# Kernel tuning notes

Hardware: AMD Instinct MI355X
Metric: run time of the kernel (lower is better)

## Reference

```python
import jax, jax.numpy as jnp
import numpy as np

N_DOMAINS = 8
LN_EPS = 1e-5


def setup_inputs() -> dict:
    key = jax.random.key(0)
    ks = jax.random.split(key, 4)
    N, D_IN, D_HID, D_OUT = 32768, 256, 1024, 256
    x = jax.random.normal(ks[0], (N, D_IN), dtype=jnp.float32)
    domain_types = jax.random.randint(ks[1], (N,), 0, N_DOMAINS, dtype=jnp.int32)
    # Per-domain MLP parameters (8 independent experts)
    W1 = jax.random.normal(ks[2], (N_DOMAINS, D_IN, D_HID), dtype=jnp.float32) * (1.0 / np.sqrt(D_IN))
    b1 = jnp.zeros((N_DOMAINS, D_HID), dtype=jnp.float32)
    gamma = jnp.ones((N_DOMAINS, D_HID), dtype=jnp.float32)
    beta = jnp.zeros((N_DOMAINS, D_HID), dtype=jnp.float32)
    W2 = jax.random.normal(ks[3], (N_DOMAINS, D_HID, D_OUT), dtype=jnp.float32) * (1.0 / np.sqrt(D_HID))
    b2 = jnp.zeros((N_DOMAINS, D_OUT), dtype=jnp.float32)
    return {"x": x, "domain_types": domain_types, "W1": W1, "b1": b1,
            "gamma": gamma, "beta": beta, "W2": W2, "b2": b2}


def _expert_mlp(x, W1d, b1d, gd, bd, W2d, b2d):
    # Linear -> LayerNorm -> ReLU -> (Dropout: identity at eval) -> Linear
    h = x @ W1d + b1d                       # [N, hid]
    mu = jnp.mean(h, axis=-1, keepdims=True)
    var = jnp.mean(jnp.square(h - mu), axis=-1, keepdims=True)
    h = (h - mu) * jax.lax.rsqrt(var + LN_EPS) * gd + bd
    h = jax.nn.relu(h)
    return h @ W2d + b2d                    # [N, out]


def reference(x, domain_types, W1, b1, gamma, beta, W2, b2):
    # output dim == x.shape[-1] (as in the torch code: zeros(batch, x.shape[-1]))
    out = jnp.zeros((x.shape[0], x.shape[-1]), dtype=x.dtype)
    for d in range(N_DOMAINS):  # small fixed expert loop (static MoE dispatch)
        y = _expert_mlp(x, W1[d], b1[d], gamma[d], beta[d], W2[d], b2[d])
        mask = (domain_types == d)[:, None]
        out = jnp.where(mask, y, out)
    return out
```

## Files before the change

kernel.cpp:

```cpp
#include <hip/hip_runtime.h>
#include <hip/hip_bf16.h>


#define ND 8
#define NROWS 32768
#define DIN 256
#define DHID 1024
#define DOUT 256
#define MPAD 33792
#define NTILES 264

typedef short short8 __attribute__((ext_vector_type(8)));
typedef float floatx4 __attribute__((ext_vector_type(4)));

__device__ __forceinline__ unsigned short f2bf(float f) {
    unsigned u = __builtin_bit_cast(unsigned, f);
    unsigned r = u + 0x7fff + ((u >> 16) & 1);
    return (unsigned short)(r >> 16);
}
__device__ __forceinline__ float bf2f(unsigned short h) {
    unsigned u = ((unsigned)h) << 16;
    return __builtin_bit_cast(float, u);
}

#define GLDS16(gp, lp) __builtin_amdgcn_global_load_lds( \
    (const __attribute__((address_space(1))) void*)(gp), \
    (__attribute__((address_space(3))) void*)(lp), 16, 0, 0)

__global__ void transpose_both(const float* __restrict__ W1, unsigned short* __restrict__ W1T,
                               const float* __restrict__ W2, unsigned short* __restrict__ W2T,
                               int* __restrict__ cnt) {
    if (blockIdx.x == 0 && threadIdx.x < 16) cnt[threadIdx.x] = 0;
    __shared__ float t[32][33];
    int b = blockIdx.x;
    const float* in; unsigned short* out; int R, C, bx, by, z;
    if (b < 2048) {
        in = W1; out = W1T; R = DIN; C = DHID;
        bx = b & 31; by = (b >> 5) & 7; z = b >> 8;
    } else {
        b -= 2048;
        in = W2; out = W2T; R = DHID; C = DOUT;
        bx = b & 7; by = (b >> 3) & 31; z = b >> 8;
    }
    const int c0 = bx * 32, r0 = by * 32;
    const int tx = threadIdx.x & 31, ty = threadIdx.x >> 5;
    const float* src = in + (size_t)z * R * C;
    unsigned short* dst = out + (size_t)z * R * C;
#pragma unroll
    for (int i = 0; i < 32; i += 8)
        t[ty + i][tx] = src[(size_t)(r0 + ty + i) * C + c0 + tx];
    __syncthreads();
#pragma unroll
    for (int i = 0; i < 32; i += 8)
        dst[(size_t)(c0 + ty + i) * R + r0 + tx] = f2bf(t[tx][ty + i]);
}

__global__ void init_histo(const int* __restrict__ dt, int* __restrict__ perm,
                           int* __restrict__ counts) {
    const int i = blockIdx.x * 256 + threadIdx.x;
    if (i < MPAD) perm[i] = -1;
    __shared__ int lc[ND];
    if (threadIdx.x < ND) lc[threadIdx.x] = 0;
    __syncthreads();
    if (i < NROWS) atomicAdd(&lc[dt[i]], 1);
    __syncthreads();
    if (threadIdx.x < ND && lc[threadIdx.x] > 0)
        atomicAdd(&counts[threadIdx.x], lc[threadIdx.x]);
}

__global__ void make_meta(const int* __restrict__ counts, int* __restrict__ cursors,
                          int2* __restrict__ meta) {
    __shared__ int base[ND], ntc[ND];
    const int t = threadIdx.x;
    if (t == 0) {
        int off = 0;
        for (int d = 0; d < ND; d++) {
            base[d] = off;
            ntc[d] = (counts[d] + 127) >> 7;
            cursors[d] = off;
            off += ntc[d] << 7;
        }
    }
    __syncthreads();
    for (int i = t; i < NTILES; i += 64) {
        int2 m = make_int2(-1, 0);
#pragma unroll
        for (int d = 0; d < ND; d++) {
            const int ti = i - (base[d] >> 7);
            if (ti >= 0 && ti < ntc[d]) m = make_int2(d, base[d] + (ti << 7));
        }
        meta[i] = m;
    }
}

__global__ __launch_bounds__(256)
void assign_pos(const int* __restrict__ dt, int* __restrict__ cursors,
                int* __restrict__ perm, int* __restrict__ pos) {
    __shared__ int lcnt[ND];
    __shared__ int lbase[ND];
    const int tid = threadIdx.x;
    if (tid < ND) lcnt[tid] = 0;
    __syncthreads();
    const int r = blockIdx.x * 256 + tid;
    const int d = dt[r];
    const int myrank = atomicAdd(&lcnt[d], 1);
    __syncthreads();
    if (tid < ND && lcnt[tid] > 0)
        lbase[tid] = atomicAdd(&cursors[tid], lcnt[tid]);
    __syncthreads();
    const int p = lbase[d] + myrank;
    pos[r] = p;
    perm[p] = r;
}

__global__ __launch_bounds__(256)
void copy_rows(const float* __restrict__ x, const int* __restrict__ pos,
               unsigned short* __restrict__ xs) {
    const int tid = threadIdx.x;
    const int lane = tid & 63;
    const int r = blockIdx.x * 4 + (tid >> 6);
    const int p = pos[r];
    float4 v = ((const float4*)(x + (size_t)r * DIN))[lane];
    ushort4 o;
    o.x = f2bf(v.x); o.y = f2bf(v.y); o.z = f2bf(v.z); o.w = f2bf(v.w);
    ((ushort4*)(xs + (size_t)p * DIN))[lane] = o;
}

template <int K, bool ISB>
__global__ __launch_bounds__(256, 2)
void gemm_bt(const unsigned short* __restrict__ A,
             const unsigned short* __restrict__ Bt,
             const float* __restrict__ bias,
             const int2* __restrict__ meta,
             const int* __restrict__ perm,
             unsigned short* __restrict__ Cbf,
             float* __restrict__ Cf,
             const int Ntot,
             float2* __restrict__ spart,
             const float* __restrict__ gamma,
             const float* __restrict__ beta) {
    constexpr int NB = ISB ? 2 : 8;
    constexpr int NWG = NTILES * NB;
    constexpr int NS = K / 32;
    const int bid = (int)blockIdx.x;
    const int wid = (bid & 7) * (NWG >> 3) + (bid >> 3);
    const int tile = wid / NB;
    const int n0 = (wid % NB) * 128;
    const int2 md = meta[tile];
    const int dom = md.x;
    if (dom < 0) return;
    const int m0 = md.y;

    __shared__ unsigned short As[2][128 * 32];
    __shared__ unsigned short Bs[2][128 * 32];
    __shared__ float gb[ISB ? 2048 : 64];
    __shared__ float sred[2][128];

    const int tid = threadIdx.x;
    const int lane = tid & 63;
    const int w = tid >> 6;
    const int wr = w >> 1, wc = w & 1;
    const int l15 = lane & 15;

    const unsigned short* Abase = A + (size_t)m0 * K;
    const unsigned short* Bbase = Bt + (size_t)dom * Ntot * K + (size_t)n0 * K;

    if (!ISB) {
        if (tid < 128) { sred[0][tid] = 0.f; sred[1][tid] = 0.f; }
    }

    const int ma = (w * 128 + lane) >> 2;
    const int kc = lane & 3;
    float muv[2], rsv[2];
    short8 hv0{}, hv1{};
    if (ISB) {
        ((float4*)gb)[tid] = ((const float4*)(gamma + dom * DHID))[tid];
        ((float4*)(gb + 1024))[tid] = ((const float4*)(beta + dom * DHID))[tid];
#pragma unroll
        for (int h2 = 0; h2 < 2; ++h2) {
            const int rm = m0 + ma + h2 * 16;
            float s = 0.f, s2 = 0.f;
#pragma unroll
            for (int nb = 0; nb < 8; ++nb) {
                const float2 p = spart[(size_t)nb * MPAD + rm];
                s += p.x; s2 += p.y;
            }
            const float mu = s * (1.f / 1024.f);
            const float var = fmaxf(s2 * (1.f / 1024.f) - mu * mu, 0.f);
            muv[h2] = mu;
            rsv[h2] = rsqrtf(var + 1e-5f);
        }
        hv0 = *(const short8*)(Abase + (size_t)ma * K + kc * 8);
        hv1 = *(const short8*)(Abase + (size_t)(ma + 16) * K + kc * 8);
    }

#define STAGE_B(buf, t_) {                                                     \
        const int k0_ = (t_) * 32;                                             \
        _Pragma("unroll")                                                      \
        for (int it = 0; it < 2; ++it) {                                       \
            const int c = w * 128 + it * 64 + lane;                            \
            const int m_ = c >> 2, kcc = c & 3;                                \
            GLDS16(Bbase + (size_t)m_ * K + k0_ + kcc * 8,                     \
                   &Bs[buf][(w * 128 + it * 64) * 8]);                         \
        }                                                                      \
    }
#define STAGE_A_GLDS(buf, t_) {                                                \
        const int k0_ = (t_) * 32;                                             \
        _Pragma("unroll")                                                      \
        for (int it = 0; it < 2; ++it) {                                       \
            const int c = w * 128 + it * 64 + lane;                            \
            const int m_ = c >> 2, kcc = c & 3;                                \
            GLDS16(Abase + (size_t)m_ * K + k0_ + kcc * 8,                     \
                   &As[buf][(w * 128 + it * 64) * 8]);                         \
        }                                                                      \
    }
#define STAGE_A_XFRM(buf, t_) {                                                \
        const int k1 = (t_) * 32 + kc * 8;                                     \
        const float4 g0 = *(const float4*)&gb[k1];                             \
        const float4 g1 = *(const float4*)&gb[k1 + 4];                         \
        const float4 e0 = *(const float4*)&gb[1024 + k1];                      \
        const float4 e1 = *(const float4*)&gb[1024 + k1 + 4];                  \
        const float gA[8] = {g0.x, g0.y, g0.z, g0.w, g1.x, g1.y, g1.z, g1.w};  \
        const float eA[8] = {e0.x, e0.y, e0.z, e0.w, e1.x, e1.y, e1.z, e1.w};  \
        _Pragma("unroll")                                                      \
        for (int h2 = 0; h2 < 2; ++h2) {                                       \
            const float mu = muv[h2], rs = rsv[h2];                            \
            const short8 hvv = h2 ? hv1 : hv0;                                 \
            short8 o;                                                          \
            _Pragma("unroll")                                                  \
            for (int e = 0; e < 8; ++e) {                                      \
                const float rg = gA[e] * rs;                                   \
                const float v = fmaxf(fmaf(bf2f((unsigned short)hvv[e]), rg,   \
                                           fmaf(-mu, rg, eA[e])), 0.f);        \
                o[e] = (short)f2bf(v);                                         \
            }                                                                  \
            *(short8*)&As[buf][(w * 128 + h2 * 64 + lane) * 8] = o;            \
        }                                                                      \
    }
#define LOAD_H(t_) {                                                           \
        const int k0_ = (t_) * 32;                                             \
        hv0 = *(const short8*)(Abase + (size_t)ma * K + k0_ + kc * 8);         \
        hv1 = *(const short8*)(Abase + (size_t)(ma + 16) * K + k0_ + kc * 8);  \
    }

    floatx4 acc[4][4];
#pragma unroll
    for (int i = 0; i < 4; i++)
#pragma unroll
        for (int j = 0; j < 4; j++) acc[i][j] = 0.f;

    STAGE_B(0, 0)
    if (!ISB) {
        STAGE_A_GLDS(0, 0)
    } else {
        STAGE_A_XFRM(0, 0)
        LOAD_H(1)
    }
    __syncthreads();

    int cur = 0;
    const int kk = (lane >> 4) * 8;
    for (int t = 0; t < NS - 1; ++t) {
        const int nx = cur ^ 1;
        STAGE_B(nx, t + 1)
        if (!ISB) {
            STAGE_A_GLDS(nx, t + 1)
        } else {
            STAGE_A_XFRM(nx, t + 1)
            if (t + 2 < NS) LOAD_H(t + 2)
        }
        short8 a[4], b[4];
#pragma unroll
        for (int i = 0; i < 4; i++) {
            const int m = wr * 64 + i * 16 + l15;
            a[i] = *(const short8*)&As[cur][m * 32 + kk];
            const int n = wc * 64 + i * 16 + l15;
            b[i] = *(const short8*)&Bs[cur][n * 32 + kk];
        }
        __builtin_amdgcn_s_setprio(1);
#pragma unroll
        for (int i = 0; i < 4; i++)
#pragma unroll
            for (int j = 0; j < 4; j++)
                acc[i][j] = __builtin_amdgcn_mfma_f32_16x16x32_bf16(a[i], b[j], acc[i][j], 0, 0, 0);
        __builtin_amdgcn_s_setprio(0);
        __syncthreads();
        cur = nx;
    }
    {
        short8 a[4], b[4];
#pragma unroll
        for (int i = 0; i < 4; i++) {
            const int m = wr * 64 + i * 16 + l15;
            a[i] = *(const short8*)&As[cur][m * 32 + kk];
            const int n = wc * 64 + i * 16 + l15;
            b[i] = *(const short8*)&Bs[cur][n * 32 + kk];
        }
        __builtin_amdgcn_s_setprio(1);
#pragma unroll
        for (int i = 0; i < 4; i++)
#pragma unroll
            for (int j = 0; j < 4; j++)
                acc[i][j] = __builtin_amdgcn_mfma_f32_16x16x32_bf16(a[i], b[j], acc[i][j], 0, 0, 0);
        __builtin_amdgcn_s_setprio(0);
    }
#undef STAGE_B
#undef STAGE_A_GLDS
#undef STAGE_A_XFRM
#undef LOAD_H

    const int quad = lane >> 4;
    if (!ISB) {
        float bv[4];
#pragma unroll
        for (int j = 0; j < 4; j++)
            bv[j] = bias[dom * Ntot + n0 + wc * 64 + j * 16 + l15];
#pragma unroll
        for (int i = 0; i < 4; i++) {
#pragma unroll
            for (int r = 0; r < 4; r++) {
                const int rl = wr * 64 + i * 16 + quad * 4 + r;
                float s = 0.f, s2 = 0.f;
#pragma unroll
                for (int j = 0; j < 4; j++) {
                    const float v = acc[i][j][r] + bv[j];
                    Cbf[(size_t)(m0 + rl) * Ntot + n0 + wc * 64 + j * 16 + l15] = f2bf(v);
                    s += v; s2 += v * v;
                }
#pragma unroll
                for (int o = 8; o; o >>= 1) {
                    s  += __shfl_xor(s, o, 64);
                    s2 += __shfl_xor(s2, o, 64);
                }
                if (l15 == 0) {
                    atomicAdd(&sred[0][rl], s);
                    atomicAdd(&sred[1][rl], s2);
                }
            }
        }
        __syncthreads();
        if (tid < 128)
            spart[(size_t)(n0 >> 7) * MPAD + m0 + tid] =
                make_float2(sred[0][tid], sred[1][tid]);
    } else {
#pragma unroll
        for (int i = 0; i < 4; i++) {
            const int rowbase = m0 + wr * 64 + i * 16 + quad * 4;
#pragma unroll
            for (int r = 0; r < 4; r++) {
                const int orig = perm[rowbase + r];
                if (orig < 0) continue;
#pragma unroll
                for (int j = 0; j < 4; j++) {
                    const int col = n0 + wc * 64 + j * 16 + l15;
                    Cf[(size_t)orig * Ntot + col] = acc[i][j][r] + bias[dom * Ntot + col];
                }
            }
        }
    }
}

extern "C" void kernel_launch(void* const* d_in, const int* in_sizes, int n_in,
                              void* d_out, int out_size, void* d_ws, size_t ws_size,
                              hipStream_t stream) {
    const float* x = (const float*)d_in[0];
    const int* dt = (const int*)d_in[1];
    const float* W1 = (const float*)d_in[2];
    const float* b1 = (const float*)d_in[3];
    const float* gamma = (const float*)d_in[4];
    const float* beta = (const float*)d_in[5];
    const float* W2 = (const float*)d_in[6];
    const float* b2 = (const float*)d_in[7];
    float* out = (float*)d_out;

    char* ws = (char*)d_ws;
    size_t off = 0;
    auto take = [&](size_t nbytes) -> char* {
        char* p = ws + off;
        off = (off + nbytes + 255) & ~(size_t)255;
        return p;
    };
    unsigned short* W1T = (unsigned short*)take((size_t)ND * DHID * DIN * 2);
    unsigned short* W2T = (unsigned short*)take((size_t)ND * DOUT * DHID * 2);
    unsigned short* XS  = (unsigned short*)take((size_t)MPAD * DIN * 2);
    unsigned short* H   = (unsigned short*)take((size_t)MPAD * DHID * 2);
    float2* SPART = (float2*)take((size_t)8 * MPAD * 8);
    int* PERM   = (int*)take(MPAD * 4);
    int* POS    = (int*)take(NROWS * 4);
    int* CNT    = (int*)take(64);
    int2* META  = (int2*)take(NTILES * 8);
    (void)ws_size; (void)n_in; (void)in_sizes; (void)out_size;

    int* COUNTS = CNT;
    int* CURSORS = CNT + 8;

    transpose_both<<<4096, 256, 0, stream>>>(W1, W1T, W2, W2T, CNT);
    init_histo<<<MPAD / 256, 256, 0, stream>>>(dt, PERM, COUNTS);
    make_meta<<<1, 64, 0, stream>>>(COUNTS, CURSORS, META);
    assign_pos<<<NROWS / 256, 256, 0, stream>>>(dt, CURSORS, PERM, POS);
    copy_rows<<<NROWS / 4, 256, 0, stream>>>(x, POS, XS);
    gemm_bt<DIN, false><<<NTILES * 8, 256, 0, stream>>>(
        XS, W1T, b1, META, nullptr, H, nullptr, DHID, SPART, nullptr, nullptr);
    gemm_bt<DHID, true><<<NTILES * 2, 256, 0, stream>>>(
        H, W2T, b2, META, PERM, nullptr, out, DOUT, SPART, gamma, beta);
}
```

Baseline: 201.6 us.

## Fuse preprocessing into cooperative kernel and use K=64 swizzled second GEMM

The five small preprocessing kernels (weight transpose, histogram, metadata, position assignment, row copy) are merged into one cooperative kernel that uses grid-wide syncs, cutting launch overhead and the gaps between launches. The second GEMM becomes a dedicated kernel with a 64-wide K step and an XOR-swizzled LDS layout, and W2T is written pre-swizzled to match. This halves the number of K iterations and barriers and is meant to cut LDS bank conflicts. In exchange, the prep phase runs on only 256 blocks and pays for grid.sync, and the larger LDS tiles may lower occupancy.

```diff
diff --git a/kernel.cpp b/kernel.cpp
--- a/kernel.cpp
+++ b/kernel.cpp
@@ -1,6 +1,9 @@
 #include <hip/hip_runtime.h>
 #include <hip/hip_bf16.h>
-
+#include <hip/hip_cooperative_groups.h>
+
+
+namespace cg = cooperative_groups;
 
 #define ND 8
 #define NROWS 32768
@@ -27,121 +30,122 @@
     (const __attribute__((address_space(1))) void*)(gp), \
     (__attribute__((address_space(3))) void*)(lp), 16, 0, 0)
 
-__global__ void transpose_both(const float* __restrict__ W1, unsigned short* __restrict__ W1T,
-                               const float* __restrict__ W2, unsigned short* __restrict__ W2T,
-                               int* __restrict__ cnt) {
-    if (blockIdx.x == 0 && threadIdx.x < 16) cnt[threadIdx.x] = 0;
+__global__ void prep(const float* __restrict__ W1, unsigned short* __restrict__ W1T,
+                     const float* __restrict__ W2, unsigned short* __restrict__ W2T,
+                     const int* __restrict__ dt, const float* __restrict__ x,
+                     unsigned short* __restrict__ XS, int* __restrict__ perm,
+                     int* __restrict__ pos, int* __restrict__ cnt,
+                     int2* __restrict__ meta) {
+    cg::grid_group grid = cg::this_grid();
     __shared__ float t[32][33];
-    int b = blockIdx.x;
-    const float* in; unsigned short* out; int R, C, bx, by, z;
-    if (b < 2048) {
-        in = W1; out = W1T; R = DIN; C = DHID;
-        bx = b & 31; by = (b >> 5) & 7; z = b >> 8;
-    } else {
-        b -= 2048;
-        in = W2; out = W2T; R = DHID; C = DOUT;
-        bx = b & 7; by = (b >> 3) & 31; z = b >> 8;
-    }
-    const int c0 = bx * 32, r0 = by * 32;
-    const int tx = threadIdx.x & 31, ty = threadIdx.x >> 5;
-    const float* src = in + (size_t)z * R * C;
-    unsigned short* dst = out + (size_t)z * R * C;
-#pragma unroll
-    for (int i = 0; i < 32; i += 8)
-        t[ty + i][tx] = src[(size_t)(r0 + ty + i) * C + c0 + tx];
-    __syncthreads();
-#pragma unroll
-    for (int i = 0; i < 32; i += 8)
-        dst[(size_t)(c0 + ty + i) * R + r0 + tx] = f2bf(t[tx][ty + i]);
-}
-
-__global__ void init_histo(const int* __restrict__ dt, int* __restrict__ perm,
-                           int* __restrict__ counts) {
-    const int i = blockIdx.x * 256 + threadIdx.x;
-    if (i < MPAD) perm[i] = -1;
-    __shared__ int lc[ND];
-    if (threadIdx.x < ND) lc[threadIdx.x] = 0;
-    __syncthreads();
-    if (i < NROWS) atomicAdd(&lc[dt[i]], 1);
-    __syncthreads();
-    if (threadIdx.x < ND && lc[threadIdx.x] > 0)
-        atomicAdd(&counts[threadIdx.x], lc[threadIdx.x]);
-}
-
-__global__ void make_meta(const int* __restrict__ counts, int* __restrict__ cursors,
-                          int2* __restrict__ meta) {
+    __shared__ int lc[ND], lb[ND];
     __shared__ int base[ND], ntc[ND];
-    const int t = threadIdx.x;
-    if (t == 0) {
-        int off = 0;
-        for (int d = 0; d < ND; d++) {
-            base[d] = off;
-            ntc[d] = (counts[d] + 127) >> 7;
-            cursors[d] = off;
-            off += ntc[d] << 7;
-        }
-    }
-    __syncthreads();
-    for (int i = t; i < NTILES; i += 64) {
-        int2 m = make_int2(-1, 0);
-#pragma unroll
-        for (int d = 0; d < ND; d++) {
-            const int ti = i - (base[d] >> 7);
-            if (ti >= 0 && ti < ntc[d]) m = make_int2(d, base[d] + (ti << 7));
-        }
-        meta[i] = m;
-    }
-}
-
-__global__ __launch_bounds__(256)
-void assign_pos(const int* __restrict__ dt, int* __restrict__ cursors,
-                int* __restrict__ perm, int* __restrict__ pos) {
-    __shared__ int lcnt[ND];
-    __shared__ int lbase[ND];
     const int tid = threadIdx.x;
-    if (tid < ND) lcnt[tid] = 0;
-    __syncthreads();
-    const int r = blockIdx.x * 256 + tid;
-    const int d = dt[r];
-    const int myrank = atomicAdd(&lcnt[d], 1);
-    __syncthreads();
-    if (tid < ND && lcnt[tid] > 0)
-        lbase[tid] = atomicAdd(&cursors[tid], lcnt[tid]);
-    __syncthreads();
-    const int p = lbase[d] + myrank;
-    pos[r] = p;
-    perm[p] = r;
-}
-
-__global__ __launch_bounds__(256)
-void copy_rows(const float* __restrict__ x, const int* __restrict__ pos,
-               unsigned short* __restrict__ xs) {
-    const int tid = threadIdx.x;
-    const int lane = tid & 63;
-    const int r = blockIdx.x * 4 + (tid >> 6);
-    const int p = pos[r];
-    float4 v = ((const float4*)(x + (size_t)r * DIN))[lane];
-    ushort4 o;
-    o.x = f2bf(v.x); o.y = f2bf(v.y); o.z = f2bf(v.z); o.w = f2bf(v.w);
-    ((ushort4*)(xs + (size_t)p * DIN))[lane] = o;
-}
-
-template <int K, bool ISB>
+    const int bid = blockIdx.x;
+
+    if (bid == 0 && tid < 16) cnt[tid] = 0;
+    {
+        const int i = bid * 256 + tid;
+        if (i < MPAD) perm[i] = -1;
+    }
+    const int tx = tid & 31, ty = tid >> 5;
+    for (int job = bid; job < 4096; job += 256) {
+        const float* in; unsigned short* out; int R, C, bx, by, z, is2;
+        if (job < 2048) { in = W1; out = W1T; R = DIN;  C = DHID; is2 = 0;
+                          bx = job & 31; by = (job >> 5) & 7;  z = job >> 8; }
+        else { const int j2 = job - 2048;
+               in = W2; out = W2T; R = DHID; C = DOUT; is2 = 1;
+               bx = j2 & 7;  by = (j2 >> 3) & 31; z = j2 >> 8; }
+        const int c0 = bx * 32, r0 = by * 32;
+        const float* src = in + (size_t)z * R * C;
+        unsigned short* dst = out + (size_t)z * R * C;
+#pragma unroll
+        for (int i = 0; i < 32; i += 8)
+            t[ty + i][tx] = src[(size_t)(r0 + ty + i) * C + c0 + tx];
+        __syncthreads();
+#pragma unroll
+        for (int i = 0; i < 32; i += 8) {
+            const int row = c0 + ty + i;
+            int k = r0 + tx;
+            if (is2)
+                k = (k & ~0x38) | (((((k >> 3) & 7) ^ (row & 7))) << 3);
+            dst[(size_t)row * R + k] = f2bf(t[tx][ty + i]);
+        }
+        __syncthreads();
+    }
+    grid.sync();
+
+    if (tid < ND) lc[tid] = 0;
+    __syncthreads();
+    if (bid < 128) {
+        atomicAdd(&lc[dt[bid * 256 + tid]], 1);
+    }
+    __syncthreads();
+    if (bid < 128 && tid < ND && lc[tid] > 0) atomicAdd(&cnt[tid], lc[tid]);
+    grid.sync();
+
+    if (bid == 0) {
+        if (tid == 0) {
+            int off = 0;
+            for (int d = 0; d < ND; d++) {
+                base[d] = off;
+                ntc[d] = (cnt[d] + 127) >> 7;
+                cnt[8 + d] = off;
+                off += ntc[d] << 7;
+            }
+        }
+        __syncthreads();
+        for (int i = tid; i < NTILES; i += 256) {
+            int2 m = make_int2(-1, 0);
+#pragma unroll
+            for (int d = 0; d < ND; d++) {
+                const int ti = i - (base[d] >> 7);
+                if (ti >= 0 && ti < ntc[d]) m = make_int2(d, base[d] + (ti << 7));
+            }
+            meta[i] = m;
+        }
+    }
+    grid.sync();
+
+    if (bid < 128) {
+        if (tid < ND) lc[tid] = 0;
+        __syncthreads();
+        const int r = bid * 256 + tid;
+        const int d = dt[r];
+        const int myrank = atomicAdd(&lc[d], 1);
+        __syncthreads();
+        if (tid < ND && lc[tid] > 0)
+            lb[tid] = atomicAdd(&cnt[8 + tid], lc[tid]);
+        __syncthreads();
+        const int p = lb[d] + myrank;
+        pos[r] = p;
+        perm[p] = r;
+    }
+    grid.sync();
+
+    {
+        const int g = bid * 256 + tid;
+#pragma unroll 4
+        for (int k = 0; k < 32; ++k) {
+            const int idx = g + k * 65536;
+            const int row = idx >> 6, c = idx & 63;
+            const int p = pos[row];
+            const float4 v = ((const float4*)(x + (size_t)row * DIN))[c];
+            ushort4 o;
+            o.x = f2bf(v.x); o.y = f2bf(v.y); o.z = f2bf(v.z); o.w = f2bf(v.w);
+            ((ushort4*)(XS + (size_t)p * DIN))[c] = o;
+        }
+    }
+}
+
 __global__ __launch_bounds__(256, 2)
-void gemm_bt(const unsigned short* __restrict__ A,
-             const unsigned short* __restrict__ Bt,
-             const float* __restrict__ bias,
-             const int2* __restrict__ meta,
-             const int* __restrict__ perm,
-             unsigned short* __restrict__ Cbf,
-             float* __restrict__ Cf,
-             const int Ntot,
-             float2* __restrict__ spart,
-             const float* __restrict__ gamma,
-             const float* __restrict__ beta) {
-    constexpr int NB = ISB ? 2 : 8;
-    constexpr int NWG = NTILES * NB;
-    constexpr int NS = K / 32;
+void gemm_a(const unsigned short* __restrict__ A,
+            const unsigned short* __restrict__ Bt,
+            const float* __restrict__ bias,
+            const int2* __restrict__ meta,
+            unsigned short* __restrict__ Cbf,
+            float2* __restrict__ spart) {
+    constexpr int K = DIN, Ntot = DHID, NB = 8, NWG = NTILES * NB, NS = K / 32;
     const int bid = (int)blockIdx.x;
     const int wid = (bid & 7) * (NWG >> 3) + (bid >> 3);
     const int tile = wid / NB;
@@ -153,7 +157,6 @@
 
     __shared__ unsigned short As[2][128 * 32];
     __shared__ unsigned short Bs[2][128 * 32];
-    __shared__ float gb[ISB ? 2048 : 64];
     __shared__ float sred[2][128];
 
     const int tid = threadIdx.x;
@@ -165,36 +168,9 @@
     const unsigned short* Abase = A + (size_t)m0 * K;
     const unsigned short* Bbase = Bt + (size_t)dom * Ntot * K + (size_t)n0 * K;
 
-    if (!ISB) {
-        if (tid < 128) { sred[0][tid] = 0.f; sred[1][tid] = 0.f; }
-    }
-
-    const int ma = (w * 128 + lane) >> 2;
-    const int kc = lane & 3;
-    float muv[2], rsv[2];
-    short8 hv0{}, hv1{};
-    if (ISB) {
-        ((float4*)gb)[tid] = ((const float4*)(gamma + dom * DHID))[tid];
-        ((float4*)(gb + 1024))[tid] = ((const float4*)(beta + dom * DHID))[tid];
-#pragma unroll
-        for (int h2 = 0; h2 < 2; ++h2) {
-            const int rm = m0 + ma + h2 * 16;
-            float s = 0.f, s2 = 0.f;
-#pragma unroll
-            for (int nb = 0; nb < 8; ++nb) {
-                const float2 p = spart[(size_t)nb * MPAD + rm];
-                s += p.x; s2 += p.y;
-            }
-            const float mu = s * (1.f / 1024.f);
-            const float var = fmaxf(s2 * (1.f / 1024.f) - mu * mu, 0.f);
-            muv[h2] = mu;
-            rsv[h2] = rsqrtf(var + 1e-5f);
-        }
-        hv0 = *(const short8*)(Abase + (size_t)ma * K + kc * 8);
-        hv1 = *(const short8*)(Abase + (size_t)(ma + 16) * K + kc * 8);
-    }
-
-#define STAGE_B(buf, t_) {                                                     \
+    if (tid < 128) { sred[0][tid] = 0.f; sred[1][tid] = 0.f; }
+
+#define STAGE_AB(buf, t_) {                                                    \
         const int k0_ = (t_) * 32;                                             \
         _Pragma("unroll")                                                      \
         for (int it = 0; it < 2; ++it) {                                       \
@@ -202,46 +178,10 @@
             const int m_ = c >> 2, kcc = c & 3;                                \
             GLDS16(Bbase + (size_t)m_ * K + k0_ + kcc * 8,                     \
                    &Bs[buf][(w * 128 + it * 64) * 8]);                         \
-        }                                                                      \
-    }
-#define STAGE_A_GLDS(buf, t_) {                                                \
-        const int k0_ = (t_) * 32;                                             \
-        _Pragma("unroll")                                                      \
-        for (int it = 0; it < 2; ++it) {                                       \
-            const int c = w * 128 + it * 64 + lane;                            \
-            const int m_ = c >> 2, kcc = c & 3;                                \
             GLDS16(Abase + (size_t)m_ * K + k0_ + kcc * 8,                     \
                    &As[buf][(w * 128 + it * 64) * 8]);                         \
         }                                                                      \
     }
-#define STAGE_A_XFRM(buf, t_) {                                                \
-        const int k1 = (t_) * 32 + kc * 8;                                     \
-        const float4 g0 = *(const float4*)&gb[k1];                             \
-        const float4 g1 = *(const float4*)&gb[k1 + 4];                         \
-        const float4 e0 = *(const float4*)&gb[1024 + k1];                      \
-        const float4 e1 = *(const float4*)&gb[1024 + k1 + 4];                  \
-        const float gA[8] = {g0.x, g0.y, g0.z, g0.w, g1.x, g1.y, g1.z, g1.w};  \
-        const float eA[8] = {e0.x, e0.y, e0.z, e0.w, e1.x, e1.y, e1.z, e1.w};  \
-        _Pragma("unroll")                                                      \
-        for (int h2 = 0; h2 < 2; ++h2) {                                       \
-            const float mu = muv[h2], rs = rsv[h2];                            \
-            const short8 hvv = h2 ? hv1 : hv0;                                 \
-            short8 o;                                                          \
-            _Pragma("unroll")                                                  \
-            for (int e = 0; e < 8; ++e) {                                      \
-                const float rg = gA[e] * rs;                                   \
-                const float v = fmaxf(fmaf(bf2f((unsigned short)hvv[e]), rg,   \
-                                           fmaf(-mu, rg, eA[e])), 0.f);        \
-                o[e] = (short)f2bf(v);                                         \
-            }                                                                  \
-            *(short8*)&As[buf][(w * 128 + h2 * 64 + lane) * 8] = o;            \
-        }                                                                      \
-    }
-#define LOAD_H(t_) {                                                           \
-        const int k0_ = (t_) * 32;                                             \
-        hv0 = *(const short8*)(Abase + (size_t)ma * K + k0_ + kc * 8);         \
-        hv1 = *(const short8*)(Abase + (size_t)(ma + 16) * K + k0_ + kc * 8);  \
-    }
 
     floatx4 acc[4][4];
 #pragma unroll
@@ -249,26 +189,14 @@
 #pragma unroll
         for (int j = 0; j < 4; j++) acc[i][j] = 0.f;
 
-    STAGE_B(0, 0)
-    if (!ISB) {
-        STAGE_A_GLDS(0, 0)
-    } else {
-        STAGE_A_XFRM(0, 0)
-        LOAD_H(1)
-    }
+    STAGE_AB(0, 0)
     __syncthreads();
 
     int cur = 0;
     const int kk = (lane >> 4) * 8;
     for (int t = 0; t < NS - 1; ++t) {
         const int nx = cur ^ 1;
-        STAGE_B(nx, t + 1)
-        if (!ISB) {
-            STAGE_A_GLDS(nx, t + 1)
-        } else {
-            STAGE_A_XFRM(nx, t + 1)
-            if (t + 2 < NS) LOAD_H(t + 2)
-        }
+        STAGE_AB(nx, t + 1)
         short8 a[4], b[4];
 #pragma unroll
         for (int i = 0; i < 4; i++) {
@@ -304,57 +232,216 @@
                 acc[i][j] = __builtin_amdgcn_mfma_f32_16x16x32_bf16(a[i], b[j], acc[i][j], 0, 0, 0);
         __builtin_amdgcn_s_setprio(0);
     }
+#undef STAGE_AB
+
+    const int quad = lane >> 4;
+    float bv[4];
+#pragma unroll
+    for (int j = 0; j < 4; j++)
+        bv[j] = bias[dom * Ntot + n0 + wc * 64 + j * 16 + l15];
+#pragma unroll
+    for (int i = 0; i < 4; i++) {
+#pragma unroll
+        for (int r = 0; r < 4; r++) {
+            const int rl = wr * 64 + i * 16 + quad * 4 + r;
+            float s = 0.f, s2 = 0.f;
+#pragma unroll
+            for (int j = 0; j < 4; j++) {
+                const float v = acc[i][j][r] + bv[j];
+                Cbf[(size_t)(m0 + rl) * Ntot + n0 + wc * 64 + j * 16 + l15] = f2bf(v);
+                s += v; s2 += v * v;
+            }
+#pragma unroll
+            for (int o = 8; o; o >>= 1) {
+                s  += __shfl_xor(s, o, 64);
+                s2 += __shfl_xor(s2, o, 64);
+            }
+            if (l15 == 0) {
+                atomicAdd(&sred[0][rl], s);
+                atomicAdd(&sred[1][rl], s2);
+            }
+        }
+    }
+    __syncthreads();
+    if (tid < 128)
+        spart[(size_t)(n0 >> 7) * MPAD + m0 + tid] =
+            make_float2(sred[0][tid], sred[1][tid]);
+}
+
+__global__ __launch_bounds__(256, 2)
+void gemm_b64(const unsigned short* __restrict__ H,
+              const unsigned short* __restrict__ W2T,
+              const float* __restrict__ b2,
+              const int2* __restrict__ meta,
+              const int* __restrict__ perm,
+              float* __restrict__ out,
+              const float2* __restrict__ spart,
+              const float* __restrict__ gamma,
+              const float* __restrict__ beta) {
+    constexpr int K = DHID, NWG = NTILES * 2, NS = K / 64;
+    const int bid = (int)blockIdx.x;
+    const int wid = (bid & 7) * (NWG >> 3) + (bid >> 3);
+    const int tile = wid >> 1;
+    const int n0 = (wid & 1) * 128;
+    const int2 md = meta[tile];
+    const int dom = md.x;
+    if (dom < 0) return;
+    const int m0 = md.y;
+
+    __shared__ unsigned short As[2][128 * 64];
+    __shared__ unsigned short Bs[2][128 * 64];
+    __shared__ float gb[2048];
+
+    const int tid = threadIdx.x;
+    const int lane = tid & 63;
+    const int w = tid >> 6;
+    const int wr = w >> 1, wc = w & 1;
+    const int l15 = lane & 15;
+    const int quad = lane >> 4;
+
+    const unsigned short* Hbase = H + (size_t)m0 * K;
+    const unsigned short* Bbase = W2T + (size_t)dom * DOUT * K + (size_t)n0 * K;
+
+    ((float4*)gb)[tid] = ((const float4*)(gamma + dom * DHID))[tid];
+    ((float4*)(gb + 1024))[tid] = ((const float4*)(beta + dom * DHID))[tid];
+
+    const int ma = w * 32 + (lane >> 2);
+    const int kc = lane & 3;
+    float muv[2], rsv[2];
+#pragma unroll
+    for (int h2 = 0; h2 < 2; ++h2) {
+        const int rm = m0 + ma + h2 * 16;
+        float s = 0.f, s2 = 0.f;
+#pragma unroll
+        for (int nb = 0; nb < 8; ++nb) {
+            const float2 p = spart[(size_t)nb * MPAD + rm];
+            s += p.x; s2 += p.y;
+        }
+        const float mu = s * (1.f / 1024.f);
+        const float var = fmaxf(s2 * (1.f / 1024.f) - mu * mu, 0.f);
+        muv[h2] = mu;
+        rsv[h2] = rsqrtf(var + 1e-5f);
+    }
+
+    short8 hv[2][2];
+
+#define LOAD_H(t_) {                                                           \
+        hv[0][0] = *(const short8*)(Hbase + (size_t)ma * K + (t_) * 64 + kc * 8);        \
+        hv[0][1] = *(const short8*)(Hbase + (size_t)ma * K + (t_) * 64 + (kc + 4) * 8);  \
+        hv[1][0] = *(const short8*)(Hbase + (size_t)(ma + 16) * K + (t_) * 64 + kc * 8); \
+        hv[1][1] = *(const short8*)(Hbase + (size_t)(ma + 16) * K + (t_) * 64 + (kc + 4) * 8); }
+
+#define XFRM(buf, t_) {                                                        \
+        _Pragma("unroll")                                                      \
+        for (int r2 = 0; r2 < 2; ++r2) {                                       \
+            const int row = ma + r2 * 16;                                      \
+            const float mu = muv[r2], rs = rsv[r2];                            \
+            _Pragma("unroll")                                                  \
+            for (int c2 = 0; c2 < 2; ++c2) {                                   \
+                const int s_ = kc + c2 * 4;                                    \
+                const int k1 = (t_) * 64 + s_ * 8;                             \
+                const float4 g0 = *(const float4*)&gb[k1];                     \
+                const float4 g1 = *(const float4*)&gb[k1 + 4];                 \
+                const float4 e0 = *(const float4*)&gb[1024 + k1];              \
+                const float4 e1 = *(const float4*)&gb[1024 + k1 + 4];          \
+                const float gA[8] = {g0.x, g0.y, g0.z, g0.w,                   \
+                                     g1.x, g1.y, g1.z, g1.w};                  \
+                const float eA[8] = {e0.x, e0.y, e0.z, e0.w,                   \
+                                     e1.x, e1.y, e1.z, e1.w};                  \
+                const short8 hvv = hv[r2][c2];                                 \
+                short8 o;                                                      \
+                _Pragma("unroll")                                              \
+                for (int e = 0; e < 8; ++e) {                                  \
+                    const float rg = gA[e] * rs;                               \
+                    const float v = fmaxf(fmaf(bf2f((unsigned short)hvv[e]),   \
+                                   rg, fmaf(-mu, rg, eA[e])), 0.f);            \
+                    o[e] = (short)f2bf(v);                                     \
+                }                                                              \
+                *(short8*)&As[buf][row * 64 + ((s_ ^ (row & 7)) << 3)] = o;    \
+            }                                                                  \
+        }                                                                      \
+    }
+
+#define STAGE_B(buf, t_) {                                                     \
+        _Pragma("unroll")                                                      \
+        for (int it = 0; it < 4; ++it) {                                       \
+            const int cb = w * 256 + it * 64;                                  \
+            const int c = cb + lane;                                           \
+            const int m_ = c >> 3, j_ = c & 7;                                 \
+            GLDS16(Bbase + (size_t)m_ * K + (t_) * 64 + j_ * 8,                \
+                   &Bs[buf][cb * 8]);                                          \
+        }                                                                      \
+    }
+
+#define COMPUTE(buf) {                                                         \
+        _Pragma("unroll")                                                      \
+        for (int h = 0; h < 2; ++h) {                                          \
+            short8 a[4], b[4];                                                 \
+            _Pragma("unroll")                                                  \
+            for (int i = 0; i < 4; ++i) {                                      \
+                const int m = wr * 64 + i * 16 + l15;                          \
+                a[i] = *(const short8*)&As[buf][m * 64 +                       \
+                        (((h * 4 + quad) ^ (m & 7)) << 3)];                    \
+                const int n = wc * 64 + i * 16 + l15;                          \
+                b[i] = *(const short8*)&Bs[buf][n * 64 +                       \
+                        (((h * 4 + quad) ^ (n & 7)) << 3)];                    \
+            }                                                                  \
+            __builtin_amdgcn_s_setprio(1);                                     \
+            _Pragma("unroll")                                                  \
+            for (int i = 0; i < 4; ++i)                                        \
+                _Pragma("unroll")                                              \
+                for (int j = 0; j < 4; ++j)                                    \
+                    acc[i][j] = __builtin_amdgcn_mfma_f32_16x16x32_bf16(       \
+                        a[i], b[j], acc[i][j], 0, 0, 0);                       \
+            __builtin_amdgcn_s_setprio(0);                                     \
+        }                                                                      \
+    }
+
+    floatx4 acc[4][4];
+#pragma unroll
+    for (int i = 0; i < 4; i++)
+#pragma unroll
+        for (int j = 0; j < 4; j++) acc[i][j] = 0.f;
+
+    STAGE_B(0, 0)
+    LOAD_H(0)
+    __syncthreads();
+    XFRM(0, 0)
+    LOAD_H(1)
+    __syncthreads();
+
+    int cur = 0;
+    for (int t = 0; t < NS - 1; ++t) {
+        const int nx = cur ^ 1;
+        STAGE_B(nx, t + 1)
+        XFRM(nx, t + 1)
+        if (t + 2 < NS) LOAD_H(t + 2)
+        COMPUTE(cur)
+        __syncthreads();
+        cur = nx;
+    }
+    COMPUTE(cur)
+
+#undef LOAD_H
+#undef XFRM
 #undef STAGE_B
-#undef STAGE_A_GLDS
-#undef STAGE_A_XFRM
-#undef LOAD_H
-
-    const int quad = lane >> 4;
-    if (!ISB) {
-        float bv[4];
-#pragma unroll
-        for (int j = 0; j < 4; j++)
-            bv[j] = bias[dom * Ntot + n0 + wc * 64 + j * 16 + l15];
-#pragma unroll
-        for (int i = 0; i < 4; i++) {
-#pragma unroll
-            for (int r = 0; r < 4; r++) {
-                const int rl = wr * 64 + i * 16 + quad * 4 + r;
-                float s = 0.f, s2 = 0.f;
-#pragma unroll
-                for (int j = 0; j < 4; j++) {
-                    const float v = acc[i][j][r] + bv[j];
-                    Cbf[(size_t)(m0 + rl) * Ntot + n0 + wc * 64 + j * 16 + l15] = f2bf(v);
-                    s += v; s2 += v * v;
-                }
-#pragma unroll
-                for (int o = 8; o; o >>= 1) {
-                    s  += __shfl_xor(s, o, 64);
-                    s2 += __shfl_xor(s2, o, 64);
-                }
-                if (l15 == 0) {
-                    atomicAdd(&sred[0][rl], s);
-                    atomicAdd(&sred[1][rl], s2);
-                }
-            }
-        }
-        __syncthreads();
-        if (tid < 128)
-            spart[(size_t)(n0 >> 7) * MPAD + m0 + tid] =
-                make_float2(sred[0][tid], sred[1][tid]);
-    } else {
-#pragma unroll
-        for (int i = 0; i < 4; i++) {
-            const int rowbase = m0 + wr * 64 + i * 16 + quad * 4;
-#pragma unroll
-            for (int r = 0; r < 4; r++) {
-                const int orig = perm[rowbase + r];
-                if (orig < 0) continue;
-#pragma unroll
-                for (int j = 0; j < 4; j++) {
-                    const int col = n0 + wc * 64 + j * 16 + l15;
-                    Cf[(size_t)orig * Ntot + col] = acc[i][j][r] + bias[dom * Ntot + col];
-                }
+#undef COMPUTE
+
+    float bv[4];
+#pragma unroll
+    for (int j = 0; j < 4; j++)
+        bv[j] = b2[dom * DOUT + n0 + wc * 64 + j * 16 + l15];
+#pragma unroll
+    for (int i = 0; i < 4; i++) {
+        const int rowbase = m0 + wr * 64 + i * 16 + quad * 4;
+#pragma unroll
+        for (int r = 0; r < 4; r++) {
+            const int orig = perm[rowbase + r];
+            if (orig < 0) continue;
+#pragma unroll
+            for (int j = 0; j < 4; j++) {
+                const int col = n0 + wc * 64 + j * 16 + l15;
+                out[(size_t)orig * DOUT + col] = acc[i][j][r] + bv[j];
             }
         }
     }
@@ -391,16 +478,15 @@
     int2* META  = (int2*)take(NTILES * 8);
     (void)ws_size; (void)n_in; (void)in_sizes; (void)out_size;
 
-    int* COUNTS = CNT;
-    int* CURSORS = CNT + 8;
-
-    transpose_both<<<4096, 256, 0, stream>>>(W1, W1T, W2, W2T, CNT);
-    init_histo<<<MPAD / 256, 256, 0, stream>>>(dt, PERM, COUNTS);
-    make_meta<<<1, 64, 0, stream>>>(COUNTS, CURSORS, META);
-    assign_pos<<<NROWS / 256, 256, 0, stream>>>(dt, CURSORS, PERM, POS);
-    copy_rows<<<NROWS / 4, 256, 0, stream>>>(x, POS, XS);
-    gemm_bt<DIN, false><<<NTILES * 8, 256, 0, stream>>>(
-        XS, W1T, b1, META, nullptr, H, nullptr, DHID, SPART, nullptr, nullptr);
-    gemm_bt<DHID, true><<<NTILES * 2, 256, 0, stream>>>(
-        H, W2T, b2, META, PERM, nullptr, out, DOUT, SPART, gamma, beta);
-}
+    void* args[] = {
+        (void*)&W1, (void*)&W1T, (void*)&W2, (void*)&W2T,
+        (void*)&dt, (void*)&x, (void*)&XS, (void*)&PERM,
+        (void*)&POS, (void*)&CNT, (void*)&META
+    };
+    hipLaunchCooperativeKernel((const void*)prep, dim3(256), dim3(256),
+                               args, 0, stream);
+
+    gemm_a<<<NTILES * 8, 256, 0, stream>>>(XS, W1T, b1, META, H, SPART);
+    gemm_b64<<<NTILES * 2, 256, 0, stream>>>(H, W2T, b2, META, PERM, out,
+                                             SPART, gamma, beta);
+}
```

After: 340.3 us. 68.8% more time.
